# Kernel optimization log

Measured on AMD Instinct MI355X. Metric: run time of the kernel, lower is better.

The kernel has to match this reference:

```python
import jax, jax.numpy as jnp
import numpy as np

N = 50000
E = 800000
IN_DIM = 16
H = 128
L = 4
EDGE_DIM = 7
LN_EPS = 1e-5


def _linear_params(key, fan_in, fan_out):
    kw, kb = jax.random.split(key)
    w = jax.random.normal(kw, (fan_in, fan_out), jnp.float32) * 0.02
    b = jax.random.normal(kb, (fan_out,), jnp.float32) * 0.02
    return w, b


def setup_inputs() -> dict:
    key = jax.random.key(0)
    ks = jax.random.split(key, 20)
    x = jax.random.normal(ks[0], (N, IN_DIM), jnp.float32)
    pos = jax.random.uniform(ks[1], (N, 3), jnp.float32) * 10.0
    row = jax.random.randint(ks[2], (E,), 0, N, jnp.int32)
    # guarantee no self-loops so distance > 0 (radius_graph uses loop=False)
    off = jax.random.randint(ks[3], (E,), 1, N, jnp.int32)
    col = (row + off) % N
    edge_index = jnp.stack([row, col], axis=0)

    W_in, b_in = _linear_params(ks[4], IN_DIM, H)

    def stack_layers(kbase, fan_in, fan_out):
        ws, bs = [], []
        for l in range(L):
            w, b = _linear_params(jax.random.fold_in(kbase, l), fan_in, fan_out)
            ws.append(w); bs.append(b)
        return jnp.stack(ws), jnp.stack(bs)

    We1, be1 = stack_layers(ks[5], 2 * H + EDGE_DIM, H)
    We2, be2 = stack_layers(ks[6], H, H)
    We3, be3 = stack_layers(ks[7], H, H)
    Wn1, bn1 = stack_layers(ks[8], H + H, H)
    Wn2, bn2 = stack_layers(ks[9], H, H)
    Wn3, bn3 = stack_layers(ks[10], H, H)
    ln_g = jnp.ones((L, H), jnp.float32)
    ln_b = jnp.zeros((L, H), jnp.float32)

    return {
        'x': x, 'pos': pos, 'edge_index': edge_index,
        'W_in': W_in, 'b_in': b_in,
        'We1': We1, 'be1': be1, 'We2': We2, 'be2': be2, 'We3': We3, 'be3': be3,
        'Wn1': Wn1, 'bn1': bn1, 'Wn2': Wn2, 'bn2': bn2, 'Wn3': Wn3, 'bn3': bn3,
        'ln_g': ln_g, 'ln_b': ln_b,
    }


def reference(x, pos, edge_index, W_in, b_in, We1, be1, We2, be2, We3, be3,
              Wn1, bn1, Wn2, bn2, Wn3, bn3, ln_g, ln_b):
    n = x.shape[0]
    row, col = edge_index[0], edge_index[1]  # row=source, col=target (PyG)
    rel_pos = pos[col] - pos[row]                       # (E, 3)
    dist = jnp.linalg.norm(rel_pos, axis=1, keepdims=True)  # (E, 1)
    edge_attr = jnp.concatenate([rel_pos, dist], axis=1)    # (E, 4)

    h = x @ W_in + b_in  # (N, H)
    num_layers = We1.shape[0]
    for l in range(num_layers):
        mom = h[:, 3:6]
        rel_mom = mom[col] - mom[row]                        # (E, 3)
        ea = jnp.concatenate([edge_attr, rel_mom], axis=1)   # (E, 7)
        # PyG: x_i = x[target=col], x_j = x[source=row]; EdgeMLP concats [h_i, h_j, ea]
        m = jnp.concatenate([h[col], h[row], ea], axis=1)    # (E, 2H+7)
        m = jax.nn.relu(m @ We1[l] + be1[l])
        m = jax.nn.relu(m @ We2[l] + be2[l])
        m = m @ We3[l] + be3[l]                              # (E, H)
        agg = jax.ops.segment_sum(m, col, num_segments=n)    # scatter-add to targets
        u = jnp.concatenate([h, agg], axis=1)                # (N, 2H)
        u = jax.nn.relu(u @ Wn1[l] + bn1[l])
        u = jax.nn.relu(u @ Wn2[l] + bn2[l])
        u = u @ Wn3[l] + bn3[l]                              # (N, H)
        h = h + u
        mean = jnp.mean(h, axis=-1, keepdims=True)
        var = jnp.mean(jnp.square(h - mean), axis=-1, keepdims=True)
        h = (h - mean) * jax.lax.rsqrt(var + LN_EPS) * ln_g[l] + ln_b[l]
    return h
```

## Files before the change

kernel.cpp:

```cpp
#include <hip/hip_runtime.h>
#include <stdint.h>

#define NN 50000
#define NE 800000
#define HD 128
#define NL 4
#define EM 128
#define EB 64

typedef __bf16 bf16x8 __attribute__((ext_vector_type(8)));
typedef __bf16 bf16x4 __attribute__((ext_vector_type(4)));
typedef float  f32x4  __attribute__((ext_vector_type(4)));

__device__ __forceinline__ f32x4 mfma16(bf16x8 a, bf16x8 b, f32x4 c) {
  return __builtin_amdgcn_mfma_f32_16x16x32_bf16(a, b, c, 0, 0, 0);
}

template<int MT, int NT>
__device__ __forceinline__ void zero_acc(f32x4 (&acc)[MT][NT]) {
#pragma unroll
  for (int i = 0; i < MT; ++i)
#pragma unroll
    for (int j = 0; j < NT; ++j) acc[i][j] = f32x4{0.f, 0.f, 0.f, 0.f};
}

template<int MT, int NT, int KS>
__device__ __forceinline__ void gemm_chunk(const __bf16* A, int sa,
    const __bf16* __restrict__ Bt, int Krow, int k0,
    int m_off, int n_off, int lane, f32x4 (&acc)[MT][NT])
{
  const int arow = lane & 15;
  const int quad = lane >> 4;
  bf16x8 b[KS][NT];
#pragma unroll
  for (int ks = 0; ks < KS; ++ks)
#pragma unroll
    for (int nt = 0; nt < NT; ++nt)
      b[ks][nt] = *reinterpret_cast<const bf16x8*>(
          Bt + (size_t)(n_off + nt * 16 + arow) * Krow + k0 + ks * 32 + quad * 8);
#pragma unroll
  for (int ks = 0; ks < KS; ++ks) {
    const int k = k0 + ks * 32 + quad * 8;
    bf16x8 a[MT];
#pragma unroll
    for (int mt = 0; mt < MT; ++mt)
      a[mt] = *reinterpret_cast<const bf16x8*>(A + (m_off + mt * 16 + arow) * sa + k);
#pragma unroll
    for (int mt = 0; mt < MT; ++mt)
#pragma unroll
      for (int nt = 0; nt < NT; ++nt)
        acc[mt][nt] = mfma16(a[mt], b[ks][nt], acc[mt][nt]);
  }
}

template<int MT, int NT, bool RELU>
__device__ __forceinline__ void store_tile(__bf16* O, int so,
    const float* __restrict__ bias, int m_off, int n_off, int lane,
    f32x4 (&acc)[MT][NT])
{
  const int quad = lane >> 4;
  const int cl = lane & 15;
#pragma unroll
  for (int nt = 0; nt < NT; ++nt) {
    const int col = n_off + nt * 16 + cl;
    const float bv = bias[col];
#pragma unroll
    for (int mt = 0; mt < MT; ++mt)
#pragma unroll
      for (int r = 0; r < 4; ++r) {
        const int row = m_off + mt * 16 + quad * 4 + r;
        float v = acc[mt][nt][r] + bv;
        if (RELU) v = fmaxf(v, 0.f);
        O[row * so + col] = (__bf16)v;
      }
  }
}

__global__ void prep_w(const float* __restrict__ W, __bf16* __restrict__ Wt,
                       int K0, int Kp) {
  int idx = blockIdx.x * 256 + threadIdx.x;
  int total = NL * HD * Kp;
  if (idx >= total) return;
  int l = idx / (HD * Kp);
  int rem = idx - l * HD * Kp;
  int n = rem / Kp;
  int k = rem - n * Kp;
  float v = (k < K0) ? W[((size_t)l * K0 + k) * HD + n] : 0.f;
  Wt[idx] = (__bf16)v;
}

__global__ void prep_pqw(const float* __restrict__ We1,
                         __bf16* __restrict__ Wtopt, __bf16* __restrict__ Wbott) {
  int idx = blockIdx.x * 256 + threadIdx.x;
  if (idx >= NL * HD * HD) return;
  int l = idx / (HD * HD);
  int rem = idx - l * HD * HD;
  int n = rem >> 7;
  int k = rem & 127;
  const float* W = We1 + (size_t)l * 263 * HD;
  float extra = (k >= 3 && k < 6) ? W[(260 + k - 3) * HD + n] : 0.f;
  Wtopt[idx] = (__bf16)(W[k * HD + n] + extra);
  Wbott[idx] = (__bf16)(W[(128 + k) * HD + n] - extra);
}

__global__ void h0_kernel(const float* __restrict__ x, const float* __restrict__ W,
                          const float* __restrict__ b, float* __restrict__ H32,
                          __bf16* __restrict__ HB) {
  int idx = blockIdx.x * 256 + threadIdx.x;
  if (idx >= NN * HD) return;
  int node = idx >> 7, j = idx & 127;
  const float* xr = x + node * 16;
  float s = b[j];
#pragma unroll
  for (int k = 0; k < 16; ++k) s += xr[k] * W[k * HD + j];
  H32[idx] = s;
  HB[idx] = (__bf16)s;
}

__global__ void hist_kernel(const int* __restrict__ ei, int* __restrict__ cnt) {
  int e = blockIdx.x * 256 + threadIdx.x;
  if (e < NE) atomicAdd(&cnt[ei[NE + e]], 1);
}

__global__ void scan_kernel(const int* __restrict__ cnt, int* __restrict__ cur) {
  __shared__ int wsum[16];
  __shared__ int carry;
  int t = threadIdx.x;
  int lane = t & 63, wid = t >> 6;
  if (t == 0) carry = 0;
  __syncthreads();
  for (int base = 0; base < NN; base += 1024) {
    int v = (base + t < NN) ? cnt[base + t] : 0;
    int incl = v;
#pragma unroll
    for (int off = 1; off < 64; off <<= 1) {
      int u = __shfl_up(incl, off, 64);
      if (lane >= off) incl += u;
    }
    if (lane == 63) wsum[wid] = incl;
    __syncthreads();
    int woff = 0;
    for (int k = 0; k < wid; ++k) woff += wsum[k];
    int c = carry;
    if (base + t < NN) cur[base + t] = c + woff + incl - v;
    __syncthreads();
    if (t == 1023) carry = c + woff + incl;
    __syncthreads();
  }
}

__global__ void scatter_kernel(const int* __restrict__ ei, int* __restrict__ cur,
                               int* __restrict__ ROWS, int* __restrict__ COLS) {
  int e = blockIdx.x * 256 + threadIdx.x;
  if (e < NE) {
    int r = ei[e], c = ei[NE + e];
    int p = atomicAdd(&cur[c], 1);
    ROWS[p] = r;
    COLS[p] = c;
  }
}

__global__ void dist_kernel(const float* __restrict__ pos,
                            const int* __restrict__ ROWS, const int* __restrict__ COLS,
                            __bf16* __restrict__ DSTb) {
  int p = blockIdx.x * 256 + threadIdx.x;
  if (p >= NE) return;
  int r = ROWS[p], c = COLS[p];
  float dx = pos[c * 3 + 0] - pos[r * 3 + 0];
  float dy = pos[c * 3 + 1] - pos[r * 3 + 1];
  float dz = pos[c * 3 + 2] - pos[r * 3 + 2];
  DSTb[p] = (__bf16)sqrtf(dx * dx + dy * dy + dz * dz);
}

__global__ __launch_bounds__(256, 4) void pq_kernel(
    const __bf16* __restrict__ HB, const float* __restrict__ pos,
    const __bf16* __restrict__ Wtopt, const __bf16* __restrict__ Wbott,
    const float* __restrict__ W4xyz,
    const float* __restrict__ be1,
    __bf16* __restrict__ PB, __bf16* __restrict__ QB)
{
  const int task = blockIdx.x * 4 + (threadIdx.x >> 6);
  const int lane = threadIdx.x & 63;
  const int g = task & 1;
  const int base = (task >> 1) * 32;
  if (base >= NN) return;
  const int arow = lane & 15, quad = lane >> 4, cl = lane & 15;

  const __bf16* Wt = g ? Wbott : Wtopt;
  __bf16* O = g ? QB : PB;
  f32x4 acc[2][8];
  zero_acc(acc);
#pragma unroll
  for (int ks = 0; ks < 4; ++ks) {
    const int k = ks * 32 + quad * 8;
    bf16x8 b[8];
#pragma unroll
    for (int nt = 0; nt < 8; ++nt)
      b[nt] = *reinterpret_cast<const bf16x8*>(Wt + (size_t)(nt * 16 + arow) * HD + k);
    bf16x8 a[2];
#pragma unroll
    for (int mt = 0; mt < 2; ++mt) {
      int row = base + mt * 16 + arow;
      if (row >= NN) row = NN - 1;
      a[mt] = *reinterpret_cast<const bf16x8*>(HB + (size_t)row * HD + k);
    }
#pragma unroll
    for (int mt = 0; mt < 2; ++mt)
#pragma unroll
      for (int nt = 0; nt < 8; ++nt)
        acc[mt][nt] = mfma16(a[mt], b[nt], acc[mt][nt]);
  }
  float px[2][4], py[2][4], pz[2][4];
#pragma unroll
  for (int mt = 0; mt < 2; ++mt)
#pragma unroll
    for (int r = 0; r < 4; ++r) {
      int row = base + mt * 16 + quad * 4 + r;
      if (row >= NN) row = NN - 1;
      px[mt][r] = pos[row * 3 + 0];
      py[mt][r] = pos[row * 3 + 1];
      pz[mt][r] = pos[row * 3 + 2];
    }
#pragma unroll
  for (int nt = 0; nt < 8; ++nt) {
    const int col = nt * 16 + cl;
    const float w0 = W4xyz[col], w1 = W4xyz[HD + col], w2 = W4xyz[2 * HD + col];
    const float bb = g ? 0.f : be1[col];
#pragma unroll
    for (int mt = 0; mt < 2; ++mt)
#pragma unroll
      for (int r = 0; r < 4; ++r) {
        const int row = base + mt * 16 + quad * 4 + r;
        if (row < NN) {
          float dot = px[mt][r] * w0 + py[mt][r] * w1 + pz[mt][r] * w2;
          float v = acc[mt][nt][r] + (g ? -dot : dot) + bb;
          O[(size_t)row * HD + col] = (__bf16)v;
        }
      }
  }
}

__global__ __launch_bounds__(256, 5) void edge_kernel(
    const __bf16* __restrict__ PB, const __bf16* __restrict__ QB,
    const __bf16* __restrict__ DSTb,
    const int* __restrict__ ROWS, const int* __restrict__ COLS,
    const float* __restrict__ w4d,
    const __bf16* __restrict__ We2t, const __bf16* __restrict__ We3t,
    const float* __restrict__ be2, const float* __restrict__ be3,
    float* __restrict__ AGG)
{
  __shared__ __bf16 S[EB * 136];
  __shared__ float w4ds[HD], be2s[HD], be3s[HD];
  __shared__ int colS[EB];
  const int t = threadIdx.x;
  const int base = blockIdx.x * EB;

  if (t < HD) { w4ds[t] = w4d[t]; be2s[t] = be2[t]; be3s[t] = be3[t]; }
  if (t < EB) colS[t] = COLS[base + t];
  __syncthreads();

  {
    const int i = t >> 2, cg = t & 3;
    const int p = base + i;
    const int c = colS[i];
    const int r = ROWS[p];
    const float dist = (float)DSTb[p];
    const __bf16* Prow = PB + (size_t)c * HD;
    const __bf16* Qrow = QB + (size_t)r * HD;
#pragma unroll
    for (int u = 0; u < 4; ++u) {
      const int ch = cg * 4 + u;
      bf16x8 pv = *reinterpret_cast<const bf16x8*>(Prow + ch * 8);
      bf16x8 qv = *reinterpret_cast<const bf16x8*>(Qrow + ch * 8);
      bf16x8 o;
#pragma unroll
      for (int j = 0; j < 8; ++j) {
        const int col = ch * 8 + j;
        float f = (float)pv[j] + (float)qv[j] + dist * w4ds[col];
        o[j] = (__bf16)fmaxf(f, 0.f);
      }
      *reinterpret_cast<bf16x8*>(S + i * 136 + ch * 8) = o;
    }
  }
  __syncthreads();

  const int w = t >> 6, lane = t & 63;
  const int m_off = (w >> 1) * 32, n_off = (w & 1) * 64;
  const int arow = lane & 15, quad = lane >> 4, cl = lane & 15;

  f32x4 acc[2][4];
#pragma unroll
  for (int g = 0; g < 2; ++g) {
    const __bf16* Wt = g ? We3t : We2t;
    const float* bs = g ? be3s : be2s;
    zero_acc(acc);
#pragma unroll
    for (int half = 0; half < 2; ++half) {
      bf16x8 b[2][4];
#pragma unroll
      for (int ks = 0; ks < 2; ++ks)
#pragma unroll
        for (int nt = 0; nt < 4; ++nt)
          b[ks][nt] = *reinterpret_cast<const bf16x8*>(
              Wt + (size_t)(n_off + nt * 16 + arow) * HD + half * 64 + ks * 32 + quad * 8);
#pragma unroll
      for (int ks = 0; ks < 2; ++ks) {
        const int k = half * 64 + ks * 32 + quad * 8;
        bf16x8 a[2];
#pragma unroll
        for (int mt = 0; mt < 2; ++mt)
          a[mt] = *reinterpret_cast<const bf16x8*>(S + (m_off + mt * 16 + arow) * 136 + k);
#pragma unroll
        for (int mt = 0; mt < 2; ++mt)
#pragma unroll
          for (int nt = 0; nt < 4; ++nt)
            acc[mt][nt] = mfma16(a[mt], b[ks][nt], acc[mt][nt]);
      }
    }
    __syncthreads();
#pragma unroll
    for (int nt = 0; nt < 4; ++nt) {
      const int col = n_off + nt * 16 + cl;
      const float bv = bs[col];
#pragma unroll
      for (int mt = 0; mt < 2; ++mt)
#pragma unroll
        for (int r = 0; r < 4; ++r) {
          const int row = m_off + mt * 16 + quad * 4 + r;
          float v = acc[mt][nt][r] + bv;
          if (!g) v = fmaxf(v, 0.f);
          S[row * 136 + col] = (__bf16)v;
        }
    }
    __syncthreads();
  }

  {
    const int j = t & 127, hh = t >> 7;
    const int i0 = hh * 32, i1 = i0 + 32;
    float s = 0.f;
    for (int i = i0; i < i1; ++i) {
      s += (float)S[i * 136 + j];
      const int c = colS[i];
      if (i == i1 - 1 || colS[i + 1] != c) {
        atomicAdd(&AGG[(size_t)c * HD + j], s);
        s = 0.f;
      }
    }
  }
}

__global__ __launch_bounds__(256, 2) void node_kernel(
    const __bf16* __restrict__ HBin, const float* __restrict__ AGG,
    const __bf16* __restrict__ Wn1t, const __bf16* __restrict__ Wn2t,
    const __bf16* __restrict__ Wn3t,
    const float* __restrict__ bn1, const float* __restrict__ bn2,
    const float* __restrict__ bn3,
    const float* __restrict__ lng, const float* __restrict__ lnb,
    float* __restrict__ H32, __bf16* __restrict__ HBout,
    float* __restrict__ dout)
{
  __shared__ float SB[EM * 136];
  __shared__ float ps[EM][2], psq[EM][2];
  __shared__ float mean_s[EM], rstd_s[EM];
  __bf16* B16 = reinterpret_cast<__bf16*>(SB);
  const int t = threadIdx.x;
  const int base = blockIdx.x * EM;

  {
    const int i0 = t >> 4, s = t & 15;
#pragma unroll
    for (int g = 0; g < EM / 16; ++g) {
      const int i = g * 16 + i0;
      const int node = base + i;
      uint4 v = make_uint4(0, 0, 0, 0);
      if (node < NN) v = *(reinterpret_cast<const uint4*>(HBin + (size_t)node * HD) + s);
      *reinterpret_cast<uint4*>(&B16[i * 264 + s * 8]) = v;
    }
  }
  for (int idx = t; idx < EM * 32; idx += 256) {
    const int i = idx >> 5, c4 = idx & 31;
    const int node = base + i;
    float4 v = make_float4(0.f, 0.f, 0.f, 0.f);
    if (node < NN) v = *reinterpret_cast<const float4*>(AGG + (size_t)node * HD + c4 * 4);
    __bf16* d = &B16[i * 264 + HD + c4 * 4];
    d[0] = (__bf16)v.x; d[1] = (__bf16)v.y; d[2] = (__bf16)v.z; d[3] = (__bf16)v.w;
  }
  __syncthreads();

  const int w = t >> 6, lane = t & 63;
  const int m_off = (w >> 1) * 64, n_off = (w & 1) * 64;
  f32x4 acc[4][4];
  __bf16* reg0 = B16;
  __bf16* reg1 = B16 + EM * 136;

  zero_acc(acc);
  gemm_chunk<4, 4, 4>(B16, 264, Wn1t, 256, 0,   m_off, n_off, lane, acc);
  gemm_chunk<4, 4, 4>(B16, 264, Wn1t, 256, 128, m_off, n_off, lane, acc);
  __syncthreads();
  store_tile<4, 4, true>(reg0, 136, bn1, m_off, n_off, lane, acc);
  __syncthreads();
  zero_acc(acc);
  gemm_chunk<4, 4, 4>(reg0, 136, Wn2t, 128, 0, m_off, n_off, lane, acc);
  store_tile<4, 4, true>(reg1, 136, bn2, m_off, n_off, lane, acc);
  __syncthreads();
  zero_acc(acc);
  gemm_chunk<4, 4, 4>(reg1, 136, Wn3t, 128, 0, m_off, n_off, lane, acc);
  __syncthreads();

  {
    const int quad = lane >> 4, cl = lane & 15;
#pragma unroll
    for (int nt = 0; nt < 4; ++nt) {
      const int col = n_off + nt * 16 + cl;
      const float bv = bn3[col];
#pragma unroll
      for (int mt = 0; mt < 4; ++mt)
#pragma unroll
        for (int r = 0; r < 4; ++r) {
          const int row = m_off + mt * 16 + quad * 4 + r;
          const int node = base + row;
          float hv = (node < NN) ? H32[(size_t)node * HD + col] : 0.f;
          SB[row * 136 + col] = hv + acc[mt][nt][r] + bv;
        }
    }
  }
  __syncthreads();
  {
    const int r = t >> 1, hh = t & 1;
    float s = 0.f, sq = 0.f;
    for (int j = hh * 64; j < hh * 64 + 64; ++j) {
      float v = SB[r * 136 + j];
      s += v; sq += v * v;
    }
    ps[r][hh] = s; psq[r][hh] = sq;
  }
  __syncthreads();
  if (t < EM) {
    float s = ps[t][0] + ps[t][1];
    float sq = psq[t][0] + psq[t][1];
    float mean = s * (1.f / HD);
    float var = sq * (1.f / HD) - mean * mean;
    mean_s[t] = mean;
    rstd_s[t] = rsqrtf(var + 1e-5f);
  }
  __syncthreads();
  for (int idx = t; idx < EM * HD; idx += 256) {
    const int r = idx >> 7, j = idx & 127;
    const int node = base + r;
    if (node < NN) {
      float v = (SB[r * 136 + j] - mean_s[r]) * rstd_s[r] * lng[j] + lnb[j];
      H32[(size_t)node * HD + j] = v;
      HBout[(size_t)node * HD + j] = (__bf16)v;
      if (dout) dout[(size_t)node * HD + j] = v;
    }
  }
}

extern "C" void kernel_launch(void* const* d_in, const int* in_sizes, int n_in,
                              void* d_out, int out_size, void* d_ws, size_t ws_size,
                              hipStream_t stream)
{
  const float* x    = (const float*)d_in[0];
  const float* pos  = (const float*)d_in[1];
  const int*   ei   = (const int*)d_in[2];
  const float* W_in = (const float*)d_in[3];
  const float* b_in = (const float*)d_in[4];
  const float* We1  = (const float*)d_in[5];
  const float* be1  = (const float*)d_in[6];
  const float* We2  = (const float*)d_in[7];
  const float* be2  = (const float*)d_in[8];
  const float* We3  = (const float*)d_in[9];
  const float* be3  = (const float*)d_in[10];
  const float* Wn1  = (const float*)d_in[11];
  const float* bn1  = (const float*)d_in[12];
  const float* Wn2  = (const float*)d_in[13];
  const float* bn2  = (const float*)d_in[14];
  const float* Wn3  = (const float*)d_in[15];
  const float* bn3  = (const float*)d_in[16];
  const float* lng  = (const float*)d_in[17];
  const float* lnb  = (const float*)d_in[18];
  float* out = (float*)d_out;

  char* ws = (char*)d_ws;
  size_t off = 0;
  auto alloc = [&](size_t bytes) -> char* {
    char* p = ws + off;
    off += (bytes + 255) & ~(size_t)255;
    return p;
  };
  __bf16* Wtopt = (__bf16*)alloc((size_t)NL * HD * HD * 2);
  __bf16* Wbott = (__bf16*)alloc((size_t)NL * HD * HD * 2);
  __bf16* We2t = (__bf16*)alloc((size_t)NL * HD * HD * 2);
  __bf16* We3t = (__bf16*)alloc((size_t)NL * HD * HD * 2);
  __bf16* Wn1t = (__bf16*)alloc((size_t)NL * HD * 256 * 2);
  __bf16* Wn2t = (__bf16*)alloc((size_t)NL * HD * HD * 2);
  __bf16* Wn3t = (__bf16*)alloc((size_t)NL * HD * HD * 2);
  __bf16* DSTb = (__bf16*)alloc((size_t)NE * 2);
  float*  H32  = (float*) alloc((size_t)NN * HD * 4);
  __bf16* HB   = (__bf16*)alloc((size_t)NN * HD * 2);
  __bf16* PB   = (__bf16*)alloc((size_t)NN * HD * 2);
  __bf16* QB   = (__bf16*)alloc((size_t)NN * HD * 2);
  float*  AGG  = (float*) alloc((size_t)NN * HD * 4);
  int*    CNT  = (int*)   alloc((size_t)NN * 4);
  int*    CUR  = (int*)   alloc((size_t)NN * 4);
  int*    ROWS = (int*)   alloc((size_t)NE * 4);
  int*    COLS = (int*)   alloc((size_t)NE * 4);

  hipMemsetAsync(CNT, 0, (size_t)NN * 4, stream);
  prep_pqw<<<(NL * HD * HD + 255) / 256, 256, 0, stream>>>(We1, Wtopt, Wbott);
  prep_w<<<(NL * HD * HD + 255) / 256, 256, 0, stream>>>(We2, We2t, 128, 128);
  prep_w<<<(NL * HD * HD + 255) / 256, 256, 0, stream>>>(We3, We3t, 128, 128);
  prep_w<<<(NL * HD * 256 + 255) / 256, 256, 0, stream>>>(Wn1, Wn1t, 256, 256);
  prep_w<<<(NL * HD * HD + 255) / 256, 256, 0, stream>>>(Wn2, Wn2t, 128, 128);
  prep_w<<<(NL * HD * HD + 255) / 256, 256, 0, stream>>>(Wn3, Wn3t, 128, 128);
  h0_kernel<<<(NN * HD + 255) / 256, 256, 0, stream>>>(x, W_in, b_in, H32, HB);
  hist_kernel<<<(NE + 255) / 256, 256, 0, stream>>>(ei, CNT);
  scan_kernel<<<1, 1024, 0, stream>>>(CNT, CUR);
  scatter_kernel<<<(NE + 255) / 256, 256, 0, stream>>>(ei, CUR, ROWS, COLS);
  dist_kernel<<<(NE + 255) / 256, 256, 0, stream>>>(pos, ROWS, COLS, DSTb);

  const int pq_tasks = 2 * ((NN + 31) / 32);
  const int pq_blocks = (pq_tasks + 3) / 4;
  for (int l = 0; l < NL; ++l) {
    const float* We1l = We1 + (size_t)l * 263 * HD;
    pq_kernel<<<pq_blocks, 256, 0, stream>>>(HB, pos,
        Wtopt + (size_t)l * HD * HD, Wbott + (size_t)l * HD * HD,
        We1l + 256 * HD,
        be1 + l * HD, PB, QB);
    hipMemsetAsync(AGG, 0, (size_t)NN * HD * 4, stream);
    edge_kernel<<<NE / EB, 256, 0, stream>>>(PB, QB, DSTb, ROWS, COLS,
        We1l + 259 * HD,
        We2t + (size_t)l * HD * HD, We3t + (size_t)l * HD * HD,
        be2 + l * HD, be3 + l * HD, AGG);
    node_kernel<<<(NN + EM - 1) / EM, 256, 0, stream>>>(HB, AGG,
        Wn1t + (size_t)l * HD * 256, Wn2t + (size_t)l * HD * HD,
        Wn3t + (size_t)l * HD * HD,
        bn1 + l * HD, bn2 + l * HD, bn3 + l * HD,
        lng + l * HD, lnb + l * HD,
        H32, HB, (l == NL - 1) ? out : nullptr);
  }
}
```

Baseline: 1.514 ms.

## Process two edge tiles per block with prefetch; shrink node tile to 64 rows

The edge kernel now handles two 64-edge tiles per block. It loads the second tile's gathered P/Q rows into registers before the first tile's GEMMs, so the gather latency overlaps with MFMA work, and it uses a second shared buffer for that tile. The node kernel drops from 128-row to 64-row blocks with a 1x8 wave tiling and launch bounds raised to 4 blocks per CU. The aim is more blocks for occupancy, at the cost of more register pressure in the edge kernel.

```diff
diff --git a/kernel.cpp b/kernel.cpp
--- a/kernel.cpp
+++ b/kernel.cpp
@@ -5,7 +5,7 @@
 #define NE 800000
 #define HD 128
 #define NL 4
-#define EM 128
+#define NM 64
 #define EB 64
 
 typedef __bf16 bf16x8 __attribute__((ext_vector_type(8)));
@@ -240,7 +240,7 @@
   }
 }
 
-__global__ __launch_bounds__(256, 5) void edge_kernel(
+__global__ __launch_bounds__(256, 4) void edge_kernel(
     const __bf16* __restrict__ PB, const __bf16* __restrict__ QB,
     const __bf16* __restrict__ DSTb,
     const int* __restrict__ ROWS, const int* __restrict__ COLS,
@@ -249,21 +249,22 @@
     const float* __restrict__ be2, const float* __restrict__ be3,
     float* __restrict__ AGG)
 {
-  __shared__ __bf16 S[EB * 136];
+  __shared__ __bf16 T0s[EB * 136];
+  __shared__ __bf16 T1s[EB * 136];
   __shared__ float w4ds[HD], be2s[HD], be3s[HD];
-  __shared__ int colS[EB];
+  __shared__ int colS[2 * EB];
   const int t = threadIdx.x;
-  const int base = blockIdx.x * EB;
+  const int base = blockIdx.x * (2 * EB);
 
   if (t < HD) { w4ds[t] = w4d[t]; be2s[t] = be2[t]; be3s[t] = be3[t]; }
-  if (t < EB) colS[t] = COLS[base + t];
-  __syncthreads();
-
+  if (t < 2 * EB) colS[t] = COLS[base + t];
+  __syncthreads();
+
+  const int i = t >> 2, cg = t & 3;
   {
-    const int i = t >> 2, cg = t & 3;
     const int p = base + i;
+    const int r = ROWS[p];
     const int c = colS[i];
-    const int r = ROWS[p];
     const float dist = (float)DSTb[p];
     const __bf16* Prow = PB + (size_t)c * HD;
     const __bf16* Qrow = QB + (size_t)r * HD;
@@ -276,10 +277,25 @@
 #pragma unroll
       for (int j = 0; j < 8; ++j) {
         const int col = ch * 8 + j;
-        float f = (float)pv[j] + (float)qv[j] + dist * w4ds[col];
-        o[j] = (__bf16)fmaxf(f, 0.f);
-      }
-      *reinterpret_cast<bf16x8*>(S + i * 136 + ch * 8) = o;
+        o[j] = (__bf16)fmaxf((float)pv[j] + (float)qv[j] + dist * w4ds[col], 0.f);
+      }
+      *reinterpret_cast<bf16x8*>(T0s + i * 136 + ch * 8) = o;
+    }
+  }
+  bf16x8 pv1[4], qv1[4];
+  float dist1;
+  {
+    const int p = base + EB + i;
+    const int r = ROWS[p];
+    const int c = colS[EB + i];
+    dist1 = (float)DSTb[p];
+    const __bf16* Prow = PB + (size_t)c * HD;
+    const __bf16* Qrow = QB + (size_t)r * HD;
+#pragma unroll
+    for (int u = 0; u < 4; ++u) {
+      const int ch = cg * 4 + u;
+      pv1[u] = *reinterpret_cast<const bf16x8*>(Prow + ch * 8);
+      qv1[u] = *reinterpret_cast<const bf16x8*>(Qrow + ch * 8);
     }
   }
   __syncthreads();
@@ -287,12 +303,9 @@
   const int w = t >> 6, lane = t & 63;
   const int m_off = (w >> 1) * 32, n_off = (w & 1) * 64;
   const int arow = lane & 15, quad = lane >> 4, cl = lane & 15;
-
   f32x4 acc[2][4];
-#pragma unroll
-  for (int g = 0; g < 2; ++g) {
-    const __bf16* Wt = g ? We3t : We2t;
-    const float* bs = g ? be3s : be2s;
+
+  auto gemm_read_mfma = [&](const __bf16* S, const __bf16* Wt) {
     zero_acc(acc);
 #pragma unroll
     for (int half = 0; half < 2; ++half) {
@@ -317,7 +330,8 @@
             acc[mt][nt] = mfma16(a[mt], b[ks][nt], acc[mt][nt]);
       }
     }
-    __syncthreads();
+  };
+  auto store_acc = [&](__bf16* S, const float* bs, bool relu) {
 #pragma unroll
     for (int nt = 0; nt < 4; ++nt) {
       const int col = n_off + nt * 16 + cl;
@@ -328,29 +342,59 @@
         for (int r = 0; r < 4; ++r) {
           const int row = m_off + mt * 16 + quad * 4 + r;
           float v = acc[mt][nt][r] + bv;
-          if (!g) v = fmaxf(v, 0.f);
+          if (relu) v = fmaxf(v, 0.f);
           S[row * 136 + col] = (__bf16)v;
         }
     }
-    __syncthreads();
-  }
-
-  {
+  };
+  auto reduce_tile = [&](const __bf16* S, const int* cseg) {
     const int j = t & 127, hh = t >> 7;
     const int i0 = hh * 32, i1 = i0 + 32;
     float s = 0.f;
-    for (int i = i0; i < i1; ++i) {
-      s += (float)S[i * 136 + j];
-      const int c = colS[i];
-      if (i == i1 - 1 || colS[i + 1] != c) {
+    for (int ii = i0; ii < i1; ++ii) {
+      s += (float)S[ii * 136 + j];
+      const int c = cseg[ii];
+      if (ii == i1 - 1 || cseg[ii + 1] != c) {
         atomicAdd(&AGG[(size_t)c * HD + j], s);
         s = 0.f;
       }
     }
-  }
-}
-
-__global__ __launch_bounds__(256, 2) void node_kernel(
+  };
+
+  gemm_read_mfma(T0s, We2t);
+  __syncthreads();
+  store_acc(T0s, be2s, true);
+  {
+#pragma unroll
+    for (int u = 0; u < 4; ++u) {
+      const int ch = cg * 4 + u;
+      bf16x8 o;
+#pragma unroll
+      for (int j = 0; j < 8; ++j) {
+        const int col = ch * 8 + j;
+        o[j] = (__bf16)fmaxf((float)pv1[u][j] + (float)qv1[u][j] + dist1 * w4ds[col], 0.f);
+      }
+      *reinterpret_cast<bf16x8*>(T1s + i * 136 + ch * 8) = o;
+    }
+  }
+  __syncthreads();
+  gemm_read_mfma(T0s, We3t);
+  __syncthreads();
+  store_acc(T0s, be3s, false);
+  __syncthreads();
+  reduce_tile(T0s, colS);
+  gemm_read_mfma(T1s, We2t);
+  __syncthreads();
+  store_acc(T1s, be2s, true);
+  __syncthreads();
+  gemm_read_mfma(T1s, We3t);
+  __syncthreads();
+  store_acc(T1s, be3s, false);
+  __syncthreads();
+  reduce_tile(T1s, colS + EB);
+}
+
+__global__ __launch_bounds__(256, 4) void node_kernel(
     const __bf16* __restrict__ HBin, const float* __restrict__ AGG,
     const __bf16* __restrict__ Wn1t, const __bf16* __restrict__ Wn2t,
     const __bf16* __restrict__ Wn3t,
@@ -360,17 +404,17 @@
     float* __restrict__ H32, __bf16* __restrict__ HBout,
     float* __restrict__ dout)
 {
-  __shared__ float SB[EM * 136];
-  __shared__ float ps[EM][2], psq[EM][2];
-  __shared__ float mean_s[EM], rstd_s[EM];
+  __shared__ float SB[NM * 136];
+  __shared__ float ps[NM][2], psq[NM][2];
+  __shared__ float mean_s[NM], rstd_s[NM];
   __bf16* B16 = reinterpret_cast<__bf16*>(SB);
   const int t = threadIdx.x;
-  const int base = blockIdx.x * EM;
+  const int base = blockIdx.x * NM;
 
   {
     const int i0 = t >> 4, s = t & 15;
 #pragma unroll
-    for (int g = 0; g < EM / 16; ++g) {
+    for (int g = 0; g < NM / 16; ++g) {
       const int i = g * 16 + i0;
       const int node = base + i;
       uint4 v = make_uint4(0, 0, 0, 0);
@@ -378,7 +422,7 @@
       *reinterpret_cast<uint4*>(&B16[i * 264 + s * 8]) = v;
     }
   }
-  for (int idx = t; idx < EM * 32; idx += 256) {
+  for (int idx = t; idx < NM * 32; idx += 256) {
     const int i = idx >> 5, c4 = idx & 31;
     const int node = base + i;
     float4 v = make_float4(0.f, 0.f, 0.f, 0.f);
@@ -389,44 +433,46 @@
   __syncthreads();
 
   const int w = t >> 6, lane = t & 63;
-  const int m_off = (w >> 1) * 64, n_off = (w & 1) * 64;
-  f32x4 acc[4][4];
+  const int m_off = w * 16, n_off = 0;
+  f32x4 acc[1][8];
   __bf16* reg0 = B16;
-  __bf16* reg1 = B16 + EM * 136;
+  __bf16* reg1 = B16 + NM * 136;
 
   zero_acc(acc);
-  gemm_chunk<4, 4, 4>(B16, 264, Wn1t, 256, 0,   m_off, n_off, lane, acc);
-  gemm_chunk<4, 4, 4>(B16, 264, Wn1t, 256, 128, m_off, n_off, lane, acc);
-  __syncthreads();
-  store_tile<4, 4, true>(reg0, 136, bn1, m_off, n_off, lane, acc);
+  gemm_chunk<1, 8, 2>(B16, 264, Wn1t, 256, 0,   m_off, n_off, lane, acc);
+  gemm_chunk<1, 8, 2>(B16, 264, Wn1t, 256, 64,  m_off, n_off, lane, acc);
+  gemm_chunk<1, 8, 2>(B16, 264, Wn1t, 256, 128, m_off, n_off, lane, acc);
+  gemm_chunk<1, 8, 2>(B16, 264, Wn1t, 256, 192, m_off, n_off, lane, acc);
+  __syncthreads();
+  store_tile<1, 8, true>(reg0, 136, bn1, m_off, n_off, lane, acc);
   __syncthreads();
   zero_acc(acc);
-  gemm_chunk<4, 4, 4>(reg0, 136, Wn2t, 128, 0, m_off, n_off, lane, acc);
-  store_tile<4, 4, true>(reg1, 136, bn2, m_off, n_off, lane, acc);
+  gemm_chunk<1, 8, 2>(reg0, 136, Wn2t, 128, 0,  m_off, n_off, lane, acc);
+  gemm_chunk<1, 8, 2>(reg0, 136, Wn2t, 128, 64, m_off, n_off, lane, acc);
+  store_tile<1, 8, true>(reg1, 136, bn2, m_off, n_off, lane, acc);
   __syncthreads();
   zero_acc(acc);
-  gemm_chunk<4, 4, 4>(reg1, 136, Wn3t, 128, 0, m_off, n_off, lane, acc);
+  gemm_chunk<1, 8, 2>(reg1, 136, Wn3t, 128, 0,  m_off, n_off, lane, acc);
+  gemm_chunk<1, 8, 2>(reg1, 136, Wn3t, 128, 64, m_off, n_off, lane, acc);
   __syncthreads();
 
   {
     const int quad = lane >> 4, cl = lane & 15;
 #pragma unroll
-    for (int nt = 0; nt < 4; ++nt) {
-      const int col = n_off + nt * 16 + cl;
+    for (int nt = 0; nt < 8; ++nt) {
+      const int col = nt * 16 + cl;
       const float bv = bn3[col];
 #pragma unroll
-      for (int mt = 0; mt < 4; ++mt)
-#pragma unroll
-        for (int r = 0; r < 4; ++r) {
-          const int row = m_off + mt * 16 + quad * 4 + r;
-          const int node = base + row;
-          float hv = (node < NN) ? H32[(size_t)node * HD + col] : 0.f;
-          SB[row * 136 + col] = hv + acc[mt][nt][r] + bv;
-        }
-    }
-  }
-  __syncthreads();
-  {
+      for (int r = 0; r < 4; ++r) {
+        const int row = m_off + quad * 4 + r;
+        const int node = base + row;
+        float hv = (node < NN) ? H32[(size_t)node * HD + col] : 0.f;
+        SB[row * 136 + col] = hv + acc[0][nt][r] + bv;
+      }
+    }
+  }
+  __syncthreads();
+  if (t < 128) {
     const int r = t >> 1, hh = t & 1;
     float s = 0.f, sq = 0.f;
     for (int j = hh * 64; j < hh * 64 + 64; ++j) {
@@ -436,7 +482,7 @@
     ps[r][hh] = s; psq[r][hh] = sq;
   }
   __syncthreads();
-  if (t < EM) {
+  if (t < NM) {
     float s = ps[t][0] + ps[t][1];
     float sq = psq[t][0] + psq[t][1];
     float mean = s * (1.f / HD);
@@ -445,7 +491,7 @@
     rstd_s[t] = rsqrtf(var + 1e-5f);
   }
   __syncthreads();
-  for (int idx = t; idx < EM * HD; idx += 256) {
+  for (int idx = t; idx < NM * HD; idx += 256) {
     const int r = idx >> 7, j = idx & 127;
     const int node = base + r;
     if (node < NN) {
@@ -529,11 +575,11 @@
         We1l + 256 * HD,
         be1 + l * HD, PB, QB);
     hipMemsetAsync(AGG, 0, (size_t)NN * HD * 4, stream);
-    edge_kernel<<<NE / EB, 256, 0, stream>>>(PB, QB, DSTb, ROWS, COLS,
+    edge_kernel<<<NE / (2 * EB), 256, 0, stream>>>(PB, QB, DSTb, ROWS, COLS,
         We1l + 259 * HD,
         We2t + (size_t)l * HD * HD, We3t + (size_t)l * HD * HD,
         be2 + l * HD, be3 + l * HD, AGG);
-    node_kernel<<<(NN + EM - 1) / EM, 256, 0, stream>>>(HB, AGG,
+    node_kernel<<<(NN + NM - 1) / NM, 256, 0, stream>>>(HB, AGG,
         Wn1t + (size_t)l * HD * 256, Wn2t + (size_t)l * HD * HD,
         Wn3t + (size_t)l * HD * HD,
         bn1 + l * HD, bn2 + l * HD, bn3 + l * HD,
```

Result: slower. 1.663 ms (+9.8%).
